# Optimization experiments

Hardware: AMD Instinct MI355X
Metric: run time of the kernel (lower is better)

## Reference

```python
import jax, jax.numpy as jnp
import numpy as np
from jax import lax

# LNS semantics: values are held as (sign, log_base|x|); exact conversion round-trips
# make log-domain mul/add mathematically identical to float conv/linear/relu, so the
# faithful reference is the equivalent float pipeline.

def _conv(x, w, b):
    # x: [B,C,H,W], w: [O,C,kh,kw] (torch layout), stride 1, no padding
    y = lax.conv_general_dilated(x, w, window_strides=(1, 1), padding='VALID',
                                 dimension_numbers=('NCHW', 'OIHW', 'NCHW'))
    return y + b[None, :, None, None]

def _maxpool2(x):
    return lax.reduce_window(x, -jnp.inf, lax.max,
                             window_dimensions=(1, 1, 2, 2),
                             window_strides=(1, 1, 2, 2), padding='VALID')

def setup_inputs() -> dict:
    key = jax.random.key(0)
    ks = jax.random.split(key, 9)
    s = lambda k, shape, fan: jax.random.normal(k, shape, jnp.float32) * (1.0 / np.sqrt(fan))
    return {
        'x': jax.random.normal(ks[0], (512, 1, 54, 54), jnp.float32),
        'conv1_w': s(ks[1], (32, 1, 3, 3), 9),
        'conv1_b': s(ks[2], (32,), 9),
        'conv2_w': s(ks[3], (64, 32, 3, 3), 32 * 9),
        'conv2_b': s(ks[4], (64,), 32 * 9),
        'fc1_w': s(ks[5], (128, 9216), 9216),
        'fc1_b': s(ks[6], (128,), 9216),
        'fc2_w': s(ks[7], (10, 128), 128),
        'fc2_b': s(ks[8], (10,), 128),
    }

def reference(x, conv1_w, conv1_b, conv2_w, conv2_b, fc1_w, fc1_b, fc2_w, fc2_b):
    h = jnp.maximum(_conv(x, conv1_w, conv1_b), 0.0)          # [B,32,52,52]
    h = _maxpool2(h)                                          # [B,32,26,26]
    h = jnp.maximum(_conv(h, conv2_w, conv2_b), 0.0)          # [B,64,24,24]
    h = _maxpool2(h)                                          # [B,64,12,12]
    h = h.reshape(h.shape[0], -1)                             # [B,9216]
    h = jnp.maximum(h @ fc1_w.T + fc1_b, 0.0)                 # [B,128]
    return h @ fc2_w.T + fc2_b                                # [B,10]
```

## Files before the change

kernel.cpp:

```cpp
#include <hip/hip_runtime.h>


#define B 512
#define POS 676
#define ICP 36
#define P2SZ (64*12*12)
#define SCR 26
#define IMS 58
#define IMCOPY (54 * IMS)
#define PL_USH (POS * ICP)
#define SCRATCH_USH 6656

typedef unsigned short ushort_t;
typedef ushort_t ushort4v __attribute__((ext_vector_type(4)));
typedef _Float16 f16x8 __attribute__((ext_vector_type(8)));
typedef float f32x4 __attribute__((ext_vector_type(4)));

__device__ __forceinline__ ushort_t f2h(float f) {
    union { _Float16 h; ushort_t u; } a; a.h = (_Float16)f; return a.u;
}
__device__ __forceinline__ float h2f(ushort_t u) {
    union { ushort_t u; _Float16 h; } a; a.u = u; return (float)a.h;
}

#define N_WR (64 * 9 * 32)
#define WR_BLOCKS 72
#define TR_BLOCKS 128

__global__ __launch_bounds__(256) void prep(const float* __restrict__ c2w,
                                            const float* __restrict__ f1w,
                                            ushort_t* __restrict__ wr,
                                            ushort_t* __restrict__ wfb) {
    __shared__ float tr[64 * 145];
    int blk = blockIdx.x;
    int tid = threadIdx.x;

    if (blk < WR_BLOCKS) {
        int t = blk * 256 + tid;
        int ic  = t & 31;
        int tap = (t >> 5) % 9;
        int oc  = t / 288;
        wr[t] = f2h(c2w[oc * 288 + ic * 9 + tap]);
        return;
    }
    int n = blk - WR_BLOCKS;
    const float* src = f1w + (size_t)n * 9216;
#pragma unroll
    for (int i = 0; i < 36; ++i) {
        int idx = i * 256 + tid;
        int oc = idx / 144, pos = idx - oc * 144;
        tr[oc * 145 + pos] = src[idx];
    }
    __syncthreads();
    ushort_t* dst = wfb + (size_t)n * 9216;
#pragma unroll
    for (int i = 0; i < 36; ++i) {
        int idx = i * 256 + tid;
        int pos = idx >> 6, oc = idx & 63;
        dst[idx] = f2h(tr[oc * 145 + pos]);
    }
}

__global__ __launch_bounds__(512, 4) void conv12(const float* __restrict__ x,
                                                 const float* __restrict__ w1,
                                                 const float* __restrict__ bias1,
                                                 const ushort_t* __restrict__ wr,
                                                 const float* __restrict__ bias2,
                                                 ushort_t* __restrict__ pool2cl) {
    __shared__ ushort_t smem[PL_USH + SCRATCH_USH];
    ushort_t* pl  = smem;
    ushort_t* img = smem + PL_USH;

    int b   = blockIdx.x;
    int tid = threadIdx.x;
    int lane = tid & 63, wid = tid >> 6;
    int quad = lane >> 4, lr = lane & 15;

    for (int i = tid; i < 54; i += 512) {
        ushort_t* r0 = img + i * IMS;
        r0[54] = 0; r0[55] = 0; r0[56] = 0; r0[57] = 0;
        ushort_t* r1 = img + IMCOPY + i * IMS;
        r1[53] = 0; r1[54] = 0; r1[55] = 0; r1[56] = 0; r1[57] = 0;
    }
    if (tid < 96) img[2 * IMCOPY + tid] = 0;

    const float* xim = x + (size_t)b * 2916;
    for (int i = tid; i < 729; i += 512) {
        int e = i * 4;
        int r = e / 54, c = e - r * 54;
        float4 xv = *reinterpret_cast<const float4*>(&xim[e]);
        ushort_t h0 = f2h(xv.x), h1 = f2h(xv.y), h2 = f2h(xv.z), h3 = f2h(xv.w);
        if (c <= 50) {
            ushort_t* p0 = &img[r * IMS + c];
            p0[0] = h0; p0[1] = h1; p0[2] = h2; p0[3] = h3;
            ushort_t* p1 = &img[IMCOPY + r * IMS + c - 1];
            if (c > 0) p1[0] = h0;
            p1[1] = h1; p1[2] = h2; p1[3] = h3;
        } else {
            img[r * IMS + 52] = h0;
            img[r * IMS + 53] = h1;
            img[(r + 1) * IMS + 0] = h2;
            img[(r + 1) * IMS + 1] = h3;
            img[IMCOPY + r * IMS + 51] = h0;
            img[IMCOPY + r * IMS + 52] = h1;
            img[IMCOPY + (r + 1) * IMS + 0] = h3;
        }
    }

    f16x8 bfrag[2];
#pragma unroll
    for (int n = 0; n < 2; ++n) {
        union { ushort_t u[8]; f16x8 v; } bu;
#pragma unroll
        for (int j = 0; j < 8; ++j) bu.u[j] = 0;
        if (quad < 3) {
            const float* wp = w1 + (n * 16 + lr) * 9 + quad * 3;
            bu.u[0] = f2h(wp[0]);
            bu.u[1] = f2h(wp[1]);
            bu.u[2] = f2h(wp[2]);
        }
        bfrag[n] = bu.v;
    }
    float bv0 = bias1[lr], bv1 = bias1[16 + lr];

    __syncthreads();

    int cbase = (lr & 1) ? (IMCOPY + lr - 1) : lr;

    for (int it = 0; it < 4; ++it) {
        int py = wid + it * 8;
        if (py >= 26) break;
        int y0 = 2 * py;
#pragma unroll
        for (int t = 0; t < 4; ++t) {
            int x0 = t * 16;
            int off0 = cbase + x0 + (y0 + quad) * IMS;
            int off1 = off0 + IMS;
            union { unsigned d[4]; f16x8 v; } a0, a1;
            a0.d[0] = *reinterpret_cast<const unsigned*>(&img[off0]);
            a0.d[1] = *reinterpret_cast<const unsigned*>(&img[off0 + 2]);
            a0.d[2] = a0.d[0]; a0.d[3] = a0.d[1];
            a1.d[0] = *reinterpret_cast<const unsigned*>(&img[off1]);
            a1.d[1] = *reinterpret_cast<const unsigned*>(&img[off1 + 2]);
            a1.d[2] = a1.d[0]; a1.d[3] = a1.d[1];

            f32x4 cA0 = (f32x4){0.f,0.f,0.f,0.f}, cA1 = cA0, cB0 = cA0, cB1 = cA0;
            cA0 = __builtin_amdgcn_mfma_f32_16x16x32_f16(a0.v, bfrag[0], cA0, 0, 0, 0);
            cA1 = __builtin_amdgcn_mfma_f32_16x16x32_f16(a0.v, bfrag[1], cA1, 0, 0, 0);
            cB0 = __builtin_amdgcn_mfma_f32_16x16x32_f16(a1.v, bfrag[0], cB0, 0, 0, 0);
            cB1 = __builtin_amdgcn_mfma_f32_16x16x32_f16(a1.v, bfrag[1], cB1, 0, 0, 0);

            if (t < 3 || quad == 0) {
                int px0 = t * 8 + quad * 2;
                float u0 = fmaxf(fmaxf(cA0[0], cA0[1]), fmaxf(cB0[0], cB0[1]));
                float u1 = fmaxf(fmaxf(cA0[2], cA0[3]), fmaxf(cB0[2], cB0[3]));
                float v0 = fmaxf(fmaxf(cA1[0], cA1[1]), fmaxf(cB1[0], cB1[1]));
                float v1 = fmaxf(fmaxf(cA1[2], cA1[3]), fmaxf(cB1[2], cB1[3]));
                ushort_t* po = pl + (py * 26 + px0) * ICP;
                po[lr]            = f2h(fmaxf(u0 + bv0, 0.0f));
                po[16 + lr]       = f2h(fmaxf(v0 + bv1, 0.0f));
                po[ICP + lr]      = f2h(fmaxf(u1 + bv0, 0.0f));
                po[ICP + 16 + lr] = f2h(fmaxf(v1 + bv1, 0.0f));
            }
        }
    }

    __syncthreads();

    int prow  = wid >> 1;
    int nhalf = wid & 1;
    const ushort_t* wb = wr + (size_t)(nhalf * 32 + lr) * 288 + quad * 8;

    int ocl = lane & 31;
    int pxh = lane >> 5;
    int oc  = nhalf * 32 + ocl;
    float bv = bias2[oc];
    ushort_t* scr = smem + PL_USH + wid * (32 * SCR);

    for (int cc = 0; cc < 3; ++cc) {
        int ebase[3];
#pragma unroll
        for (int t = 0; t < 3; ++t) {
            int m  = t * 16 + lr;
            int yl = m / 24;
            int xx = m - yl * 24;
            ebase[t] = ((8 * cc + 2 * prow + yl) * 26 + xx) * ICP + quad * 8;
        }

        f32x4 acc[3][2];
#pragma unroll
        for (int t = 0; t < 3; ++t)
#pragma unroll
            for (int n = 0; n < 2; ++n) acc[t][n] = (f32x4){0.f, 0.f, 0.f, 0.f};

#pragma unroll
        for (int tap = 0; tap < 9; ++tap) {
            int ky = tap / 3, kx = tap % 3;
            int koff = (ky * 26 + kx) * ICP;
            f16x8 a[3];
#pragma unroll
            for (int t = 0; t < 3; ++t) {
                union { ushort4v s[2]; f16x8 v; } u;
                u.s[0] = *reinterpret_cast<const ushort4v*>(&pl[ebase[t] + koff]);
                u.s[1] = *reinterpret_cast<const ushort4v*>(&pl[ebase[t] + koff + 4]);
                a[t] = u.v;
            }
            f16x8 bf[2];
#pragma unroll
            for (int n = 0; n < 2; ++n)
                bf[n] = *reinterpret_cast<const f16x8*>(wb + (size_t)n * 16 * 288 + tap * 32);
#pragma unroll
            for (int t = 0; t < 3; ++t)
#pragma unroll
                for (int n = 0; n < 2; ++n)
                    acc[t][n] = __builtin_amdgcn_mfma_f32_16x16x32_f16(a[t], bf[n], acc[t][n], 0, 0, 0);
        }

#pragma unroll
        for (int t = 0; t < 3; ++t)
#pragma unroll
            for (int n = 0; n < 2; ++n) {
                int wocl = n * 16 + lr;
                int i0 = t * 8 + quad * 2;
                float v0 = fmaxf(acc[t][n][0], acc[t][n][1]);
                float v1 = fmaxf(acc[t][n][2], acc[t][n][3]);
                union { ushort_t u2[2]; unsigned w; } pk;
                pk.u2[0] = f2h(v0); pk.u2[1] = f2h(v1);
                *reinterpret_cast<unsigned*>(&scr[wocl * SCR + i0]) = pk.w;
            }
        asm volatile("s_waitcnt lgkmcnt(0)" ::: "memory");

        const ushort_t* row = scr + ocl * SCR;
        int py = cc * 4 + prow;
        ushort_t* po = pool2cl + ((size_t)b * 144 + py * 12) * 64 + oc;
#pragma unroll
        for (int j = 0; j < 6; ++j) {
            int px = pxh * 6 + j;
            float r0 = h2f(row[px]);
            float r1 = h2f(row[px + 12]);
            po[px * 64] = f2h(fmaxf(fmaxf(r0, r1) + bv, 0.0f));
        }
        asm volatile("s_waitcnt lgkmcnt(0)" ::: "memory");
    }
}

__global__ __launch_bounds__(256) void fc1_mfma(const ushort_t* __restrict__ A,
                                                 const ushort_t* __restrict__ W,
                                                 float* __restrict__ Cpart) {
    int tid = threadIdx.x;
    int lane = tid & 63, wid = tid >> 6;
    int lr = lane & 15, quad = lane >> 4;
    int w  = blockIdx.x * 4 + wid;
    int nt = w & 3;
    int ks = (w >> 2) & 15;
    int mt = w >> 6;

    int m0 = mt * 16;
    int n0 = nt * 32;
    int k0 = ks * 576 + quad * 8;
    const ushort_t* a0 = A + (size_t)(m0 + lr) * 9216 + k0;
    const ushort_t* b0 = W + (size_t)(n0 + lr) * 9216 + k0;
    const ushort_t* b1 = b0 + (size_t)16 * 9216;

    f32x4 acc0 = (f32x4){0.f, 0.f, 0.f, 0.f};
    f32x4 acc1 = (f32x4){0.f, 0.f, 0.f, 0.f};

#pragma unroll
    for (int kk = 0; kk < 18; ++kk) {
        f16x8 av  = *reinterpret_cast<const f16x8*>(a0 + kk * 32);
        f16x8 bv0 = *reinterpret_cast<const f16x8*>(b0 + kk * 32);
        f16x8 bv1 = *reinterpret_cast<const f16x8*>(b1 + kk * 32);
        acc0 = __builtin_amdgcn_mfma_f32_16x16x32_f16(av, bv0, acc0, 0, 0, 0);
        acc1 = __builtin_amdgcn_mfma_f32_16x16x32_f16(av, bv1, acc1, 0, 0, 0);
    }

    float* cp = Cpart + (size_t)ks * (512 * 128);
    int crow = m0 + quad * 4;
#pragma unroll
    for (int r = 0; r < 4; ++r) {
        cp[(size_t)(crow + r) * 128 + n0 + lr]      = acc0[r];
        cp[(size_t)(crow + r) * 128 + n0 + 16 + lr] = acc1[r];
    }
}

__global__ __launch_bounds__(256) void fc1fc2(const float* __restrict__ Cpart,
                                              const float* __restrict__ b1,
                                              const float* __restrict__ w2,
                                              const float* __restrict__ b2,
                                              float* __restrict__ out) {
    __shared__ float h[2][128];
    int half = threadIdx.x >> 7;
    int k = threadIdx.x & 127;
    int b = blockIdx.x * 2 + half;
    float s = 0.f;
#pragma unroll
    for (int ks = 0; ks < 16; ++ks) s += Cpart[(size_t)ks * (512 * 128) + b * 128 + k];
    h[half][k] = fmaxf(s + b1[k], 0.0f);
    __syncthreads();
    if (k < 10) {
        const float* wp = w2 + k * 128;
        float acc = 0.f;
#pragma unroll 8
        for (int j = 0; j < 128; ++j) acc += h[half][j] * wp[j];
        out[b * 10 + k] = acc + b2[k];
    }
}

extern "C" void kernel_launch(void* const* d_in, const int* in_sizes, int n_in,
                              void* d_out, int out_size, void* d_ws, size_t ws_size,
                              hipStream_t stream) {
    const float* x       = (const float*)d_in[0];
    const float* conv1_w = (const float*)d_in[1];
    const float* conv1_b = (const float*)d_in[2];
    const float* conv2_w = (const float*)d_in[3];
    const float* conv2_b = (const float*)d_in[4];
    const float* fc1_w   = (const float*)d_in[5];
    const float* fc1_b   = (const float*)d_in[6];
    const float* fc2_w   = (const float*)d_in[7];
    const float* fc2_b   = (const float*)d_in[8];
    float* out = (float*)d_out;

    char* ws = (char*)d_ws;
    ushort_t* wr = (ushort_t*)ws;
    ws += N_WR * sizeof(ushort_t) + 128;
    ushort_t* wfb = (ushort_t*)ws;
    ws += (size_t)128 * 9216 * sizeof(ushort_t) + 128;
    ushort_t* pool2cl = (ushort_t*)ws;
    ws += (size_t)B * P2SZ * sizeof(ushort_t) + 128;
    float* Cpart = (float*)ws;
    ws += (size_t)16 * 512 * 128 * sizeof(float) + 128;

    prep<<<WR_BLOCKS + TR_BLOCKS, 256, 0, stream>>>(conv2_w, fc1_w, wr, wfb);
    conv12<<<B, 512, 0, stream>>>(x, conv1_w, conv1_b, wr, conv2_b, pool2cl);
    fc1_mfma<<<512, 256, 0, stream>>>(pool2cl, wfb, Cpart);
    fc1fc2<<<256, 256, 0, stream>>>(Cpart, fc1_b, fc2_w, fc2_b, out);
}
```

Baseline: 114.5 us.

## Split conv12 per image into two row-halves with halo recompute

Each image is now processed by two blocks, each handling half of the output rows: 30 input rows, 14 pooled conv1 rows and 6 pooled conv2 rows. Shared memory per block drops, and the grid doubles to 1024 blocks, so more blocks can be resident per CU and the load is spread more evenly. The cost is a 2-row halo of conv1 recomputed in each half, plus redundant input loads and weight-fragment setup per block. With cc limited to two iterations, the waves with prow >= 2 sit idle in the second pass, which leaves some imbalance.

New measurement: 118.2 us. +3.2%, slower.

```diff
diff --git a/kernel.cpp b/kernel.cpp
--- a/kernel.cpp
+++ b/kernel.cpp
@@ -7,9 +7,11 @@
 #define P2SZ (64*12*12)
 #define SCR 26
 #define IMS 58
-#define IMCOPY (54 * IMS)
-#define PL_USH (POS * ICP)
-#define SCRATCH_USH 6656
+#define IMROWS 30
+#define IMCOPY2 (IMROWS * IMS)
+#define PLROWS 14
+#define PL2_USH (PLROWS * 26 * ICP)
+#define SCRATCH2_USH 6656
 
 typedef unsigned short ushort_t;
 typedef ushort_t ushort4v __attribute__((ext_vector_type(4)));
@@ -67,25 +69,27 @@
                                                  const ushort_t* __restrict__ wr,
                                                  const float* __restrict__ bias2,
                                                  ushort_t* __restrict__ pool2cl) {
-    __shared__ ushort_t smem[PL_USH + SCRATCH_USH];
+    __shared__ ushort_t smem[PL2_USH + SCRATCH2_USH];
     ushort_t* pl  = smem;
-    ushort_t* img = smem + PL_USH;
-
-    int b   = blockIdx.x;
+    ushort_t* img = smem + PL2_USH;
+
+    int blk = blockIdx.x;
+    int b   = blk >> 1;
+    int h   = blk & 1;
     int tid = threadIdx.x;
     int lane = tid & 63, wid = tid >> 6;
     int quad = lane >> 4, lr = lane & 15;
 
-    for (int i = tid; i < 54; i += 512) {
+    for (int i = tid; i < IMROWS; i += 512) {
         ushort_t* r0 = img + i * IMS;
         r0[54] = 0; r0[55] = 0; r0[56] = 0; r0[57] = 0;
-        ushort_t* r1 = img + IMCOPY + i * IMS;
+        ushort_t* r1 = img + IMCOPY2 + i * IMS;
         r1[53] = 0; r1[54] = 0; r1[55] = 0; r1[56] = 0; r1[57] = 0;
     }
-    if (tid < 96) img[2 * IMCOPY + tid] = 0;
-
-    const float* xim = x + (size_t)b * 2916;
-    for (int i = tid; i < 729; i += 512) {
+    if (tid < 96) img[2 * IMCOPY2 + tid] = 0;
+
+    const float* xim = x + (size_t)b * 2916 + (h ? 24 * 54 : 0);
+    for (int i = tid; i < 405; i += 512) {
         int e = i * 4;
         int r = e / 54, c = e - r * 54;
         float4 xv = *reinterpret_cast<const float4*>(&xim[e]);
@@ -93,7 +97,7 @@
         if (c <= 50) {
             ushort_t* p0 = &img[r * IMS + c];
             p0[0] = h0; p0[1] = h1; p0[2] = h2; p0[3] = h3;
-            ushort_t* p1 = &img[IMCOPY + r * IMS + c - 1];
+            ushort_t* p1 = &img[IMCOPY2 + r * IMS + c - 1];
             if (c > 0) p1[0] = h0;
             p1[1] = h1; p1[2] = h2; p1[3] = h3;
         } else {
@@ -101,9 +105,9 @@
             img[r * IMS + 53] = h1;
             img[(r + 1) * IMS + 0] = h2;
             img[(r + 1) * IMS + 1] = h3;
-            img[IMCOPY + r * IMS + 51] = h0;
-            img[IMCOPY + r * IMS + 52] = h1;
-            img[IMCOPY + (r + 1) * IMS + 0] = h3;
+            img[IMCOPY2 + r * IMS + 51] = h0;
+            img[IMCOPY2 + r * IMS + 52] = h1;
+            img[IMCOPY2 + (r + 1) * IMS + 0] = h3;
         }
     }
 
@@ -125,12 +129,10 @@
 
     __syncthreads();
 
-    int cbase = (lr & 1) ? (IMCOPY + lr - 1) : lr;
-
-    for (int it = 0; it < 4; ++it) {
-        int py = wid + it * 8;
-        if (py >= 26) break;
-        int y0 = 2 * py;
+    int cbase = (lr & 1) ? (IMCOPY2 + lr - 1) : lr;
+
+    for (int py_l = wid; py_l < PLROWS; py_l += 8) {
+        int y0 = 2 * py_l;
 #pragma unroll
         for (int t = 0; t < 4; ++t) {
             int x0 = t * 16;
@@ -156,7 +158,7 @@
                 float u1 = fmaxf(fmaxf(cA0[2], cA0[3]), fmaxf(cB0[2], cB0[3]));
                 float v0 = fmaxf(fmaxf(cA1[0], cA1[1]), fmaxf(cB1[0], cB1[1]));
                 float v1 = fmaxf(fmaxf(cA1[2], cA1[3]), fmaxf(cB1[2], cB1[3]));
-                ushort_t* po = pl + (py * 26 + px0) * ICP;
+                ushort_t* po = pl + (py_l * 26 + px0) * ICP;
                 po[lr]            = f2h(fmaxf(u0 + bv0, 0.0f));
                 po[16 + lr]       = f2h(fmaxf(v0 + bv1, 0.0f));
                 po[ICP + lr]      = f2h(fmaxf(u1 + bv0, 0.0f));
@@ -175,16 +177,19 @@
     int pxh = lane >> 5;
     int oc  = nhalf * 32 + ocl;
     float bv = bias2[oc];
-    ushort_t* scr = smem + PL_USH + wid * (32 * SCR);
-
-    for (int cc = 0; cc < 3; ++cc) {
+    ushort_t* scr = smem + PL2_USH + wid * (32 * SCR);
+
+    for (int cc = 0; cc < 2; ++cc) {
+        int py2l = cc * 4 + prow;
+        if (py2l >= 6) break;
+
         int ebase[3];
 #pragma unroll
         for (int t = 0; t < 3; ++t) {
             int m  = t * 16 + lr;
             int yl = m / 24;
             int xx = m - yl * 24;
-            ebase[t] = ((8 * cc + 2 * prow + yl) * 26 + xx) * ICP + quad * 8;
+            ebase[t] = ((2 * py2l + yl) * 26 + xx) * ICP + quad * 8;
         }
 
         f32x4 acc[3][2];
@@ -231,7 +236,7 @@
         asm volatile("s_waitcnt lgkmcnt(0)" ::: "memory");
 
         const ushort_t* row = scr + ocl * SCR;
-        int py = cc * 4 + prow;
+        int py = h * 6 + py2l;
         ushort_t* po = pool2cl + ((size_t)b * 144 + py * 12) * 64 + oc;
 #pragma unroll
         for (int j = 0; j < 6; ++j) {
@@ -331,7 +336,7 @@
     ws += (size_t)16 * 512 * 128 * sizeof(float) + 128;
 
     prep<<<WR_BLOCKS + TR_BLOCKS, 256, 0, stream>>>(conv2_w, fc1_w, wr, wfb);
-    conv12<<<B, 512, 0, stream>>>(x, conv1_w, conv1_b, wr, conv2_b, pool2cl);
+    conv12<<<2 * B, 512, 0, stream>>>(x, conv1_w, conv1_b, wr, conv2_b, pool2cl);
     fc1_mfma<<<512, 256, 0, stream>>>(pool2cl, wfb, Cpart);
     fc1fc2<<<256, 256, 0, stream>>>(Cpart, fc1_b, fc2_w, fc2_b, out);
 }
```
